# Performance work log

Measured on AMD Instinct MI355X. Metric: run time of the kernel, lower is better.

The kernel has to match this reference:

```python
import jax, jax.numpy as jnp
import numpy as np

N_MIN = 5
N_MAX = 16
VARIANTS_PER_N = 16
NUM_HIDDEN = 2
HIDDEN = 512
TOTAL_MODELS = (N_MAX - N_MIN + 1) * VARIANTS_PER_N  # 192
BATCH = 65536


def setup_inputs() -> dict:
    key = jax.random.key(0)
    ks = jax.random.split(key, 8)
    n = 16
    s_in = 1.0 / np.sqrt(n)
    s_h = 1.0 / np.sqrt(HIDDEN)
    return {
        "T": jax.random.normal(ks[0], (BATCH, n), dtype=jnp.float32),
        "n": n,
        "variant_index": 3,
        "w_in": jax.random.normal(ks[1], (TOTAL_MODELS, HIDDEN, N_MAX), dtype=jnp.float32) * s_in,
        "b_in": jax.random.normal(ks[2], (TOTAL_MODELS, HIDDEN), dtype=jnp.float32) * 0.01,
        "w_hid": jax.random.normal(ks[3], (TOTAL_MODELS, NUM_HIDDEN, HIDDEN, HIDDEN), dtype=jnp.float32) * s_h,
        "b_hid": jax.random.normal(ks[4], (TOTAL_MODELS, NUM_HIDDEN, HIDDEN), dtype=jnp.float32) * 0.01,
        "w_out": jax.random.normal(ks[5], (TOTAL_MODELS, N_MAX + 1, HIDDEN), dtype=jnp.float32) * s_h,
        "b_out": jax.random.normal(ks[6], (TOTAL_MODELS, N_MAX + 1), dtype=jnp.float32) * 0.01,
    }


def _distortion(X, n):
    # X: (B, n+1). Z[:, n-1-i] = sum_j X[:, j] * X[:, j+i+1] (zero-padded shift).
    # lag k = i+1 -> column n-k; loop is over fixed small n (<=16), unrolls statically.
    cols = [jnp.sum(X[:, :-k] * X[:, k:], axis=1) for k in range(1, n + 1)]
    return jnp.stack(cols[::-1], axis=1)  # (B, n)


def reference(T, n, variant_index, w_in, b_in, w_hid, b_hid, w_out, b_out):
    model_idx = (n - N_MIN) * VARIANTS_PER_N + variant_index
    wi = w_in[model_idx]    # (H, N_MAX)
    bi = b_in[model_idx]    # (H,)
    wh = w_hid[model_idx]   # (2, H, H)
    bh = b_hid[model_idx]   # (2, H)
    wo = w_out[model_idx]   # (N_MAX+1, H)
    bo = b_out[model_idx]   # (N_MAX+1,)

    T_pad = jnp.pad(T, ((0, 0), (0, N_MAX - n)))  # (B, N_MAX)
    norm = jnp.sqrt(jnp.clip(jnp.sum(T_pad * T_pad, axis=1, keepdims=True), 1e-12))
    T_unit = T_pad / norm
    scale = jnp.sqrt(norm)

    x = jax.nn.silu(T_unit @ wi.T + bi)
    for h in range(NUM_HIDDEN):
        x = jax.nn.relu(x @ wh[h].T + bh[h])
    x_full = (x @ wo.T + bo) * scale  # (B, N_MAX+1)

    X_hat = x_full[:, :n + 1]
    X_hat_clamped = jnp.clip(X_hat, -2.0, 2.0)
    error = jnp.mean((_distortion(X_hat, n) - T) ** 2)
    error_clamped = jnp.mean((_distortion(X_hat_clamped, n) - T) ** 2)
    return (X_hat, error, X_hat_clamped, error_clamped)
```

## Files before the change

kernel.cpp:

```cpp
#include <hip/hip_runtime.h>

#define BATCH 65536
#define MT 64
#define NBLK (BATCH / MT)

typedef unsigned short u16;
typedef __bf16 bf16x8 __attribute__((ext_vector_type(8)));
typedef float f32x4 __attribute__((ext_vector_type(4)));

#define WI_OFF 0
#define WH_OFF 16384
#define WO_OFF 540672
#define WS_USH 557056
#define BI_F 0
#define BH_F 512
#define BO_F 1536
#define PART_F 1568
#define PREP_WH 65536
#define PREP_WI 2048
#define PREP_WO 2048
#define PREP_SC 1568
#define PREP_TOTAL (PREP_WH + PREP_WI + PREP_WO + PREP_SC)

__device__ inline u16 f2bf(float f) {
  union { float f; unsigned u; } v; v.f = f;
  unsigned u = v.u + 0x7fffu + ((v.u >> 16) & 1u);
  return (u16)(u >> 16);
}

__global__ void prep_kernel(const float* __restrict__ w_in, const float* __restrict__ b_in,
                            const float* __restrict__ w_hid, const float* __restrict__ b_hid,
                            const float* __restrict__ w_out, const float* __restrict__ b_out,
                            const int* __restrict__ variant, int n,
                            u16* __restrict__ wsu, float* __restrict__ wsf)
{
  const int model = (n - 5) * 16 + variant[0];
  const int i = blockIdx.x * 256 + threadIdx.x;
  if (i < PREP_WH) {
    int col = i & 511, g = (i >> 9) & 3, K32 = (i >> 11) & 15, l = i >> 15;
    const float* src = w_hid + (size_t)model * 524288 + (size_t)l * 262144 + col * 512 + K32 * 32 + g * 8;
    u16* dst = wsu + WH_OFF + (size_t)i * 8;
    #pragma unroll
    for (int e = 0; e < 8; ++e) dst[e] = f2bf(src[e]);
  } else if (i < PREP_WH + PREP_WI) {
    int j = i - PREP_WH;
    int col = j & 511, g = (j >> 9) & 3;
    u16* dst = wsu + WI_OFF + (size_t)j * 8;
    #pragma unroll
    for (int e = 0; e < 8; ++e) {
      int k = g * 8 + e;
      dst[e] = (k < 16) ? f2bf(w_in[(size_t)model * 8192 + col * 16 + k]) : (u16)0;
    }
  } else if (i < PREP_WH + PREP_WI + PREP_WO) {
    int j = i - PREP_WH - PREP_WI;
    int g = j & 3, col = (j >> 2) & 31, K32 = j >> 7;
    u16* dst = wsu + WO_OFF + (size_t)j * 8;
    #pragma unroll
    for (int e = 0; e < 8; ++e) {
      int k = K32 * 32 + g * 8 + e;
      dst[e] = (col < 17) ? f2bf(w_out[(size_t)model * 8704 + col * 512 + k]) : (u16)0;
    }
  } else if (i < PREP_TOTAL) {
    int j = i - PREP_WH - PREP_WI - PREP_WO;
    if (j < 512)       wsf[BI_F + j] = b_in[(size_t)model * 512 + j];
    else if (j < 1536) wsf[BH_F + (j - 512)] = b_hid[(size_t)model * 1024 + (j - 512)];
    else               { int o = j - 1536; wsf[BO_F + o] = (o < 17) ? b_out[(size_t)model * 17 + o] : 0.f; }
  }
}

__device__ __forceinline__ bf16x8 rdA(const char* xb, int row, int kbyte) {
  return *reinterpret_cast<const bf16x8*>(xb + row * 1024 + (kbyte ^ ((row & 15) << 4)));
}
__device__ __forceinline__ void st16(char* xb, int row, int col, u16 v) {
  *(u16*)(xb + row * 1024 + ((col * 2) ^ ((row & 15) << 4))) = v;
}

__device__ __forceinline__ void stage16(const u16* g, const u16* l) {
  __builtin_amdgcn_global_load_lds(
      (const __attribute__((address_space(1))) u16*)(uintptr_t)g,
      (__attribute__((address_space(3))) u16*)(unsigned)(uintptr_t)l,
      16, 0, 0);
}

template<int CN>
__global__ __launch_bounds__(512, 2) void fused_kernel(
    const float* __restrict__ T, const u16* __restrict__ wsu,
    const float* __restrict__ wsf, float* __restrict__ Xout, float* __restrict__ Xcout,
    float* __restrict__ errPart, int n_arg)
{
  const int n = CN ? CN : n_arg;
  __shared__ u16 xs[MT * 512];
  __shared__ u16 bs[2 * 16384];
  __shared__ float xo[MT * 20];
  __shared__ float ts[MT * 16];
  __shared__ float scaleS[MT];
  __shared__ float ered[8][2];

  const int tid = threadIdx.x;
  const int blk = blockIdx.x;
  const int lane = tid & 63;
  const int wid = tid >> 6;
  const int l15 = lane & 15;
  const int q = lane >> 4;
  const int c0 = wid * 64;
  char* xb = (char*)xs;
  char* bsB = (char*)bs;

  int bofs[4];
  #pragma unroll
  for (int ct = 0; ct < 4; ++ct)
    bofs[ct] = q * 8192 + (c0 + ct * 16 + l15) * 16;

  auto stageTile = [&](int tau) {
    if (tau > 32) return;
    const u16* src = (tau == 0) ? (wsu + WI_OFF)
                   : (tau <= 16) ? (wsu + WH_OFF + (size_t)(tau - 1) * 16384)
                                 : (wsu + WH_OFF + 262144 + (size_t)(tau - 17) * 16384);
    char* dst = bsB + ((tau & 1) << 15);
    const char* s = (const char*)src;
    #pragma unroll
    for (int c = 0; c < 4; ++c) {
      int d = tid * 16 + c * 8192;
      stage16((const u16*)(s + d), (const u16*)(dst + d));
    }
  };

  f32x4 acc[4][4];
  #pragma unroll
  for (int a = 0; a < 4; ++a)
    #pragma unroll
    for (int b = 0; b < 4; ++b) { f32x4 z = {0.f, 0.f, 0.f, 0.f}; acc[a][b] = z; }

  auto computeTile = [&](int buf, int kbA) {
    const char* bb = bsB + (buf << 15);
    bf16x8 av[4];
    #pragma unroll
    for (int mt = 0; mt < 4; ++mt) av[mt] = rdA(xb, mt * 16 + l15, kbA);
    #pragma unroll
    for (int ct = 0; ct < 4; ++ct) {
      bf16x8 b = *reinterpret_cast<const bf16x8*>(bb + bofs[ct]);
      #pragma unroll
      for (int mt = 0; mt < 4; ++mt)
        acc[mt][ct] = __builtin_amdgcn_mfma_f32_16x16x32_bf16(av[mt], b, acc[mt][ct], 0, 0, 0);
    }
  };

  auto epilogue = [&](const float* bias, int act) {
    float bv[4];
    #pragma unroll
    for (int ct = 0; ct < 4; ++ct) bv[ct] = bias[c0 + ct * 16 + l15];
    #pragma unroll
    for (int mt = 0; mt < 4; ++mt)
      #pragma unroll
      for (int ct = 0; ct < 4; ++ct) {
        #pragma unroll
        for (int j = 0; j < 4; ++j) {
          int row = mt * 16 + q * 4 + j;
          float z = acc[mt][ct][j] + bv[ct];
          float h = act ? fmaxf(z, 0.f) : z / (1.f + __expf(-z));
          st16(xb, row, c0 + ct * 16 + l15, f2bf(h));
        }
        f32x4 zz = {0.f, 0.f, 0.f, 0.f};
        acc[mt][ct] = zz;
      }
  };

  stageTile(0);
  stageTile(1);

  {
    const int r = tid >> 3, j = tid & 7;
    const size_t gr = (size_t)blk * MT + r;
    const float* tp = T + gr * n;
    const int k0 = 2 * j, k1 = 2 * j + 1;
    float v0 = (k0 < n) ? tp[k0] : 0.f;
    float v1 = (k1 < n) ? tp[k1] : 0.f;
    float ss = v0 * v0 + v1 * v1;
    ss += __shfl_xor(ss, 1); ss += __shfl_xor(ss, 2); ss += __shfl_xor(ss, 4);
    float norm = sqrtf(ss < 1e-12f ? 1e-12f : ss);
    float rn = 1.f / norm;
    if (j == 0) scaleS[r] = sqrtf(norm);
    st16(xb, r, k0, f2bf(v0 * rn));
    st16(xb, r, k1, f2bf(v1 * rn));
    st16(xb, r, 16 + k0, 0);
    st16(xb, r, 16 + k1, 0);
    ts[r * 16 + k0] = v0;
    ts[r * 16 + k1] = v1;
  }

  asm volatile("s_waitcnt vmcnt(4) lgkmcnt(0)" ::: "memory");
  __builtin_amdgcn_s_barrier();
  computeTile(0, q * 16);
  __builtin_amdgcn_s_barrier();
  stageTile(2);
  epilogue(wsf + BI_F, 0);
  asm volatile("s_waitcnt lgkmcnt(0)" ::: "memory");
  __builtin_amdgcn_s_barrier();

  #pragma unroll 1
  for (int i = 0; i < 16; ++i) {
    asm volatile("s_waitcnt vmcnt(4)" ::: "memory");
    __builtin_amdgcn_s_barrier();
    computeTile((1 + i) & 1, i * 64 + q * 16);
    __builtin_amdgcn_s_barrier();
    stageTile(3 + i);
  }
  epilogue(wsf + BH_F, 1);
  asm volatile("s_waitcnt lgkmcnt(0)" ::: "memory");
  __builtin_amdgcn_s_barrier();

  #pragma unroll 1
  for (int i = 0; i < 15; ++i) {
    asm volatile("s_waitcnt vmcnt(4)" ::: "memory");
    __builtin_amdgcn_s_barrier();
    computeTile((17 + i) & 1, i * 64 + q * 16);
    __builtin_amdgcn_s_barrier();
    stageTile(19 + i);
  }
  asm volatile("s_waitcnt vmcnt(0)" ::: "memory");
  __builtin_amdgcn_s_barrier();
  computeTile(0, 15 * 64 + q * 16);
  __builtin_amdgcn_s_barrier();
  epilogue(wsf + BH_F + 512, 1);
  asm volatile("s_waitcnt lgkmcnt(0)" ::: "memory");
  __builtin_amdgcn_s_barrier();

  {
    const int rg = wid >> 1;
    const int ch = wid & 1;
    f32x4 oacc = {0.f, 0.f, 0.f, 0.f};
    const u16* WoL = wsu + WO_OFF + (ch * 16 + l15) * 32 + q * 8;
    uint4 ob = *reinterpret_cast<const uint4*>(WoL);
    #pragma unroll 1
    for (int K = 0; K < 16; K += 2) {
      uint4 on = *reinterpret_cast<const uint4*>(WoL + (size_t)(K + 1) * 1024);
      {
        bf16x8 a0 = rdA(xb, rg * 16 + l15, K * 64 + q * 16);
        oacc = __builtin_amdgcn_mfma_f32_16x16x32_bf16(a0, __builtin_bit_cast(bf16x8, ob), oacc, 0, 0, 0);
      }
      ob = *reinterpret_cast<const uint4*>(WoL + (size_t)((K + 2) & 15) * 1024);
      {
        bf16x8 a1 = rdA(xb, rg * 16 + l15, (K + 1) * 64 + q * 16);
        oacc = __builtin_amdgcn_mfma_f32_16x16x32_bf16(a1, __builtin_bit_cast(bf16x8, on), oacc, 0, 0, 0);
      }
    }
    const int o = ch * 16 + l15;
    #pragma unroll
    for (int j = 0; j < 4; ++j) {
      int row = rg * 16 + q * 4 + j;
      if (o <= n) {
        float val = (oacc[j] + wsf[BO_F + o]) * scaleS[row];
        size_t gr = (size_t)blk * MT + row;
        float cv = fminf(fmaxf(val, -2.f), 2.f);
        Xout[gr * (n + 1) + o] = val;
        Xcout[gr * (n + 1) + o] = cv;
        xo[row * 20 + o] = val;
      }
    }
  }
  __syncthreads();

  {
    const int r = tid >> 3, j = tid & 7;
    float x[17], cx[17];
    #pragma unroll
    for (int i = 0; i < 17; ++i) {
      float v = (i <= n) ? xo[r * 20 + i] : 0.f;
      x[i] = v; cx[i] = fminf(fmaxf(v, -2.f), 2.f);
    }
    float e = 0.f, ec = 0.f;
    #pragma unroll
    for (int kk = 0; kk < 2; ++kk) {
      int k = j + 1 + kk * 8;
      if (k <= n) {
        float d = 0.f, dc = 0.f;
        #pragma unroll
        for (int i = 0; i < 16; ++i) {
          if (i + k <= 16) {
            if (i + k <= n) { d += x[i] * x[i + k]; dc += cx[i] * cx[i + k]; }
          }
        }
        float tvv = ts[r * 16 + (n - k)];
        float r1 = d - tvv, r2 = dc - tvv;
        e += r1 * r1; ec += r2 * r2;
      }
    }
    e += __shfl_xor(e, 1);  ec += __shfl_xor(ec, 1);
    e += __shfl_xor(e, 2);  ec += __shfl_xor(ec, 2);
    e += __shfl_xor(e, 4);  ec += __shfl_xor(ec, 4);
    e += __shfl_xor(e, 8);  ec += __shfl_xor(ec, 8);
    e += __shfl_xor(e, 16); ec += __shfl_xor(ec, 16);
    e += __shfl_xor(e, 32); ec += __shfl_xor(ec, 32);
    if (lane == 0) { ered[wid][0] = e; ered[wid][1] = ec; }
  }
  __syncthreads();
  if (tid == 0) {
    float e = 0.f, ec = 0.f;
    #pragma unroll
    for (int w = 0; w < 8; ++w) { e += ered[w][0]; ec += ered[w][1]; }
    errPart[blk * 2]     = e;
    errPart[blk * 2 + 1] = ec;
  }
}

__global__ void finalize_kernel(const float* __restrict__ part, float* __restrict__ e0,
                                float* __restrict__ e1, float inv)
{
  __shared__ float se[4][2];
  const int t = threadIdx.x;
  float e = 0.f, ec = 0.f;
  for (int b = t; b < NBLK; b += 256) { e += part[2 * b]; ec += part[2 * b + 1]; }
  e += __shfl_xor(e, 1);  ec += __shfl_xor(ec, 1);
  e += __shfl_xor(e, 2);  ec += __shfl_xor(ec, 2);
  e += __shfl_xor(e, 4);  ec += __shfl_xor(ec, 4);
  e += __shfl_xor(e, 8);  ec += __shfl_xor(ec, 8);
  e += __shfl_xor(e, 16); ec += __shfl_xor(ec, 16);
  e += __shfl_xor(e, 32); ec += __shfl_xor(ec, 32);
  if ((t & 63) == 0) { se[t >> 6][0] = e; se[t >> 6][1] = ec; }
  __syncthreads();
  if (t == 0) {
    float te = 0.f, tec = 0.f;
    #pragma unroll
    for (int w = 0; w < 4; ++w) { te += se[w][0]; tec += se[w][1]; }
    e0[0] = te * inv;
    e1[0] = tec * inv;
  }
}

extern "C" void kernel_launch(void* const* d_in, const int* in_sizes, int n_in,
                              void* d_out, int out_size, void* d_ws, size_t ws_size,
                              hipStream_t stream)
{
  const float* T       = (const float*)d_in[0];
  const int*   variant = (const int*)d_in[2];
  const float* w_in    = (const float*)d_in[3];
  const float* b_in    = (const float*)d_in[4];
  const float* w_hid   = (const float*)d_in[5];
  const float* b_hid   = (const float*)d_in[6];
  const float* w_out   = (const float*)d_in[7];
  const float* b_out   = (const float*)d_in[8];
  const int n = in_sizes[0] / BATCH;

  u16* wsu = (u16*)d_ws;
  float* wsf = (float*)((char*)d_ws + (size_t)WS_USH * 2);
  float* out = (float*)d_out;
  const size_t xe = (size_t)BATCH * (n + 1);
  float* Xo  = out;
  float* eP  = out + xe;
  float* Xc  = out + xe + 1;
  float* ecP = out + 2 * xe + 1;

  const int prepBlocks = (PREP_TOTAL + 255) / 256;
  prep_kernel<<<prepBlocks, 256, 0, stream>>>(w_in, b_in, w_hid, b_hid, w_out, b_out,
                                              variant, n, wsu, wsf);
  if (n == 16)
    fused_kernel<16><<<NBLK, 512, 0, stream>>>(T, wsu, wsf, Xo, Xc, wsf + PART_F, n);
  else
    fused_kernel<0><<<NBLK, 512, 0, stream>>>(T, wsu, wsf, Xo, Xc, wsf + PART_F, n);
  finalize_kernel<<<1, 256, 0, stream>>>(wsf + PART_F, eP, ecP, 1.f / (float)((size_t)BATCH * n));
}
```

Measured before the change: 134.8 us.

## Grow row tile to 96 rows to amortize weight staging per block

Raises rows per block from 64 to 96 so each staged hidden-weight tile feeds six MFMA row tiles instead of four, cutting total weight traffic and barrier overhead per row. To fit shared memory, the per-row scale is moved to a global workspace array, the output-stage scratch is aliased onto the weight staging buffer, and T is re-read from global in the distortion stage. The grid becomes 683 blocks with bounds checks for the ragged last block. The risks are higher register pressure from 24 accumulators under 2-blocks-per-SM launch bounds, a grid that fills the CUs unevenly, and extra global reads.

```diff
diff --git a/kernel.cpp b/kernel.cpp
--- a/kernel.cpp
+++ b/kernel.cpp
@@ -1,8 +1,8 @@
 #include <hip/hip_runtime.h>
 
 #define BATCH 65536
-#define MT 64
-#define NBLK (BATCH / MT)
+#define MT 96
+#define NBLK 683
 
 typedef unsigned short u16;
 typedef __bf16 bf16x8 __attribute__((ext_vector_type(8)));
@@ -15,7 +15,8 @@
 #define BI_F 0
 #define BH_F 512
 #define BO_F 1536
-#define PART_F 1568
+#define PART_F 1600
+#define SCALE_F 4096
 #define PREP_WH 65536
 #define PREP_WI 2048
 #define PREP_WO 2048
@@ -86,15 +87,11 @@
 __global__ __launch_bounds__(512, 2) void fused_kernel(
     const float* __restrict__ T, const u16* __restrict__ wsu,
     const float* __restrict__ wsf, float* __restrict__ Xout, float* __restrict__ Xcout,
-    float* __restrict__ errPart, int n_arg)
+    float* __restrict__ errPart, float* __restrict__ scaleArr, int n_arg)
 {
   const int n = CN ? CN : n_arg;
   __shared__ u16 xs[MT * 512];
   __shared__ u16 bs[2 * 16384];
-  __shared__ float xo[MT * 20];
-  __shared__ float ts[MT * 16];
-  __shared__ float scaleS[MT];
-  __shared__ float ered[8][2];
 
   const int tid = threadIdx.x;
   const int blk = blockIdx.x;
@@ -125,22 +122,22 @@
     }
   };
 
-  f32x4 acc[4][4];
+  f32x4 acc[6][4];
   #pragma unroll
-  for (int a = 0; a < 4; ++a)
+  for (int a = 0; a < 6; ++a)
     #pragma unroll
     for (int b = 0; b < 4; ++b) { f32x4 z = {0.f, 0.f, 0.f, 0.f}; acc[a][b] = z; }
 
   auto computeTile = [&](int buf, int kbA) {
     const char* bb = bsB + (buf << 15);
-    bf16x8 av[4];
-    #pragma unroll
-    for (int mt = 0; mt < 4; ++mt) av[mt] = rdA(xb, mt * 16 + l15, kbA);
+    bf16x8 av[6];
+    #pragma unroll
+    for (int mt = 0; mt < 6; ++mt) av[mt] = rdA(xb, mt * 16 + l15, kbA);
     #pragma unroll
     for (int ct = 0; ct < 4; ++ct) {
       bf16x8 b = *reinterpret_cast<const bf16x8*>(bb + bofs[ct]);
       #pragma unroll
-      for (int mt = 0; mt < 4; ++mt)
+      for (int mt = 0; mt < 6; ++mt)
         acc[mt][ct] = __builtin_amdgcn_mfma_f32_16x16x32_bf16(av[mt], b, acc[mt][ct], 0, 0, 0);
     }
   };
@@ -150,7 +147,7 @@
     #pragma unroll
     for (int ct = 0; ct < 4; ++ct) bv[ct] = bias[c0 + ct * 16 + l15];
     #pragma unroll
-    for (int mt = 0; mt < 4; ++mt)
+    for (int mt = 0; mt < 6; ++mt)
       #pragma unroll
       for (int ct = 0; ct < 4; ++ct) {
         #pragma unroll
@@ -169,23 +166,28 @@
   stageTile(1);
 
   {
-    const int r = tid >> 3, j = tid & 7;
-    const size_t gr = (size_t)blk * MT + r;
-    const float* tp = T + gr * n;
-    const int k0 = 2 * j, k1 = 2 * j + 1;
-    float v0 = (k0 < n) ? tp[k0] : 0.f;
-    float v1 = (k1 < n) ? tp[k1] : 0.f;
-    float ss = v0 * v0 + v1 * v1;
-    ss += __shfl_xor(ss, 1); ss += __shfl_xor(ss, 2); ss += __shfl_xor(ss, 4);
-    float norm = sqrtf(ss < 1e-12f ? 1e-12f : ss);
-    float rn = 1.f / norm;
-    if (j == 0) scaleS[r] = sqrtf(norm);
-    st16(xb, r, k0, f2bf(v0 * rn));
-    st16(xb, r, k1, f2bf(v1 * rn));
-    st16(xb, r, 16 + k0, 0);
-    st16(xb, r, 16 + k1, 0);
-    ts[r * 16 + k0] = v0;
-    ts[r * 16 + k1] = v1;
+    const int r = tid >> 2, j = tid & 3;
+    if (r < MT) {
+      const size_t gr = (size_t)blk * MT + r;
+      const bool valid = gr < (size_t)BATCH;
+      const float* tp = T + gr * n;
+      float v[4]; float ss = 0.f;
+      #pragma unroll
+      for (int c = 0; c < 4; ++c) {
+        int k = j * 4 + c;
+        v[c] = (valid && k < n) ? tp[k] : 0.f;
+        ss += v[c] * v[c];
+      }
+      ss += __shfl_xor(ss, 1); ss += __shfl_xor(ss, 2);
+      float norm = sqrtf(ss < 1e-12f ? 1e-12f : ss);
+      float rn = 1.f / norm;
+      if (j == 0 && valid) scaleArr[gr] = sqrtf(norm);
+      #pragma unroll
+      for (int c = 0; c < 4; ++c) {
+        st16(xb, r, j * 4 + c, f2bf(v[c] * rn));
+        st16(xb, r, 16 + j * 4 + c, 0);
+      }
+    }
   }
 
   asm volatile("s_waitcnt vmcnt(4) lgkmcnt(0)" ::: "memory");
@@ -224,65 +226,86 @@
   epilogue(wsf + BH_F + 512, 1);
   asm volatile("s_waitcnt lgkmcnt(0)" ::: "memory");
   __builtin_amdgcn_s_barrier();
+  float* xoB  = reinterpret_cast<float*>(bs);
+  float* ered = xoB + MT * 20;
+
+  if (wid < 6) {
+    f32x4 oacc[2];
+    { f32x4 z = {0.f, 0.f, 0.f, 0.f}; oacc[0] = z; oacc[1] = z; }
+    const int bofs2 = l15 * 32 + q * 8;
+    uint4 ob[2], on[2];
+    #pragma unroll
+    for (int ct = 0; ct < 2; ++ct)
+      ob[ct] = *reinterpret_cast<const uint4*>(wsu + WO_OFF + (size_t)(ct * 16) * 32 + bofs2);
+    #pragma unroll 1
+    for (int K2 = 0; K2 < 16; K2 += 2) {
+      #pragma unroll
+      for (int ct = 0; ct < 2; ++ct)
+        on[ct] = *reinterpret_cast<const uint4*>(wsu + WO_OFF + (size_t)(K2 + 1) * 1024 + (size_t)(ct * 16) * 32 + bofs2);
+      {
+        bf16x8 a = rdA(xb, wid * 16 + l15, K2 * 64 + q * 16);
+        #pragma unroll
+        for (int ct = 0; ct < 2; ++ct)
+          oacc[ct] = __builtin_amdgcn_mfma_f32_16x16x32_bf16(
+              a, __builtin_bit_cast(bf16x8, ob[ct]), oacc[ct], 0, 0, 0);
+      }
+      #pragma unroll
+      for (int ct = 0; ct < 2; ++ct)
+        ob[ct] = *reinterpret_cast<const uint4*>(wsu + WO_OFF + (size_t)((K2 + 2) & 15) * 1024 + (size_t)(ct * 16) * 32 + bofs2);
+      {
+        bf16x8 a = rdA(xb, wid * 16 + l15, (K2 + 1) * 64 + q * 16);
+        #pragma unroll
+        for (int ct = 0; ct < 2; ++ct)
+          oacc[ct] = __builtin_amdgcn_mfma_f32_16x16x32_bf16(
+              a, __builtin_bit_cast(bf16x8, on[ct]), oacc[ct], 0, 0, 0);
+      }
+    }
+    #pragma unroll
+    for (int ct = 0; ct < 2; ++ct)
+      #pragma unroll
+      for (int j = 0; j < 4; ++j) {
+        int o = ct * 16 + l15;
+        int row = wid * 16 + q * 4 + j;
+        size_t gr = (size_t)blk * MT + row;
+        if (o <= n && gr < (size_t)BATCH) {
+          float val = (oacc[ct][j] + wsf[BO_F + o]) * scaleArr[gr];
+          float cv = fminf(fmaxf(val, -2.f), 2.f);
+          Xout[gr * (n + 1) + o] = val;
+          Xcout[gr * (n + 1) + o] = cv;
+          xoB[row * 20 + o] = val;
+        }
+      }
+  }
+  __syncthreads();
 
   {
-    const int rg = wid >> 1;
-    const int ch = wid & 1;
-    f32x4 oacc = {0.f, 0.f, 0.f, 0.f};
-    const u16* WoL = wsu + WO_OFF + (ch * 16 + l15) * 32 + q * 8;
-    uint4 ob = *reinterpret_cast<const uint4*>(WoL);
-    #pragma unroll 1
-    for (int K = 0; K < 16; K += 2) {
-      uint4 on = *reinterpret_cast<const uint4*>(WoL + (size_t)(K + 1) * 1024);
-      {
-        bf16x8 a0 = rdA(xb, rg * 16 + l15, K * 64 + q * 16);
-        oacc = __builtin_amdgcn_mfma_f32_16x16x32_bf16(a0, __builtin_bit_cast(bf16x8, ob), oacc, 0, 0, 0);
-      }
-      ob = *reinterpret_cast<const uint4*>(WoL + (size_t)((K + 2) & 15) * 1024);
-      {
-        bf16x8 a1 = rdA(xb, rg * 16 + l15, (K + 1) * 64 + q * 16);
-        oacc = __builtin_amdgcn_mfma_f32_16x16x32_bf16(a1, __builtin_bit_cast(bf16x8, on), oacc, 0, 0, 0);
-      }
-    }
-    const int o = ch * 16 + l15;
-    #pragma unroll
-    for (int j = 0; j < 4; ++j) {
-      int row = rg * 16 + q * 4 + j;
-      if (o <= n) {
-        float val = (oacc[j] + wsf[BO_F + o]) * scaleS[row];
-        size_t gr = (size_t)blk * MT + row;
-        float cv = fminf(fmaxf(val, -2.f), 2.f);
-        Xout[gr * (n + 1) + o] = val;
-        Xcout[gr * (n + 1) + o] = cv;
-        xo[row * 20 + o] = val;
-      }
-    }
-  }
-  __syncthreads();
-
-  {
-    const int r = tid >> 3, j = tid & 7;
-    float x[17], cx[17];
-    #pragma unroll
-    for (int i = 0; i < 17; ++i) {
-      float v = (i <= n) ? xo[r * 20 + i] : 0.f;
-      x[i] = v; cx[i] = fminf(fmaxf(v, -2.f), 2.f);
-    }
+    const int r = tid >> 2, j = tid & 3;
     float e = 0.f, ec = 0.f;
-    #pragma unroll
-    for (int kk = 0; kk < 2; ++kk) {
-      int k = j + 1 + kk * 8;
-      if (k <= n) {
-        float d = 0.f, dc = 0.f;
-        #pragma unroll
-        for (int i = 0; i < 16; ++i) {
-          if (i + k <= 16) {
-            if (i + k <= n) { d += x[i] * x[i + k]; dc += cx[i] * cx[i + k]; }
+    if (r < MT) {
+      const size_t gr = (size_t)blk * MT + r;
+      if (gr < (size_t)BATCH) {
+        float x[17], cx[17];
+        #pragma unroll
+        for (int i = 0; i < 17; ++i) {
+          float v = (i <= n) ? xoB[r * 20 + i] : 0.f;
+          x[i] = v; cx[i] = fminf(fmaxf(v, -2.f), 2.f);
+        }
+        #pragma unroll
+        for (int kk = 0; kk < 4; ++kk) {
+          int k = j + 1 + kk * 4;
+          if (k <= n) {
+            float d = 0.f, dc = 0.f;
+            #pragma unroll
+            for (int i = 0; i < 16; ++i) {
+              if (i + k <= 16) {
+                if (i + k <= n) { d += x[i] * x[i + k]; dc += cx[i] * cx[i + k]; }
+              }
+            }
+            float tvv = T[gr * n + (n - k)];
+            float r1 = d - tvv, r2 = dc - tvv;
+            e += r1 * r1; ec += r2 * r2;
           }
         }
-        float tvv = ts[r * 16 + (n - k)];
-        float r1 = d - tvv, r2 = dc - tvv;
-        e += r1 * r1; ec += r2 * r2;
       }
     }
     e += __shfl_xor(e, 1);  ec += __shfl_xor(ec, 1);
@@ -291,13 +314,13 @@
     e += __shfl_xor(e, 8);  ec += __shfl_xor(ec, 8);
     e += __shfl_xor(e, 16); ec += __shfl_xor(ec, 16);
     e += __shfl_xor(e, 32); ec += __shfl_xor(ec, 32);
-    if (lane == 0) { ered[wid][0] = e; ered[wid][1] = ec; }
+    if (lane == 0) { ered[wid * 2] = e; ered[wid * 2 + 1] = ec; }
   }
   __syncthreads();
   if (tid == 0) {
     float e = 0.f, ec = 0.f;
     #pragma unroll
-    for (int w = 0; w < 8; ++w) { e += ered[w][0]; ec += ered[w][1]; }
+    for (int w = 0; w < 8; ++w) { e += ered[w * 2]; ec += ered[w * 2 + 1]; }
     errPart[blk * 2]     = e;
     errPart[blk * 2 + 1] = ec;
   }
@@ -354,8 +377,10 @@
   prep_kernel<<<prepBlocks, 256, 0, stream>>>(w_in, b_in, w_hid, b_hid, w_out, b_out,
                                               variant, n, wsu, wsf);
   if (n == 16)
-    fused_kernel<16><<<NBLK, 512, 0, stream>>>(T, wsu, wsf, Xo, Xc, wsf + PART_F, n);
+    fused_kernel<16><<<NBLK, 512, 0, stream>>>(T, wsu, wsf, Xo, Xc, wsf + PART_F,
+                                               wsf + SCALE_F, n);
   else
-    fused_kernel<0><<<NBLK, 512, 0, stream>>>(T, wsu, wsf, Xo, Xc, wsf + PART_F, n);
+    fused_kernel<0><<<NBLK, 512, 0, stream>>>(T, wsu, wsf, Xo, Xc, wsf + PART_F,
+                                              wsf + SCALE_F, n);
   finalize_kernel<<<1, 256, 0, stream>>>(wsf + PART_F, eP, ecP, 1.f / (float)((size_t)BATCH * n));
 }
```

Result: no change. 132.2 us (-2.0%).
